# Kernel optimization log

Measured on AMD Instinct MI355X. Metric: run time of the kernel, lower is better.

The kernel has to match this reference:

```python
import jax, jax.numpy as jnp
import numpy as np

N_EMBEDDINGS = 1024
EMBEDDING_DIM = 256
DECAY = 0.99
EPSILON = 1e-05


def setup_inputs() -> dict:
    key = jax.random.key(0)
    k1, k2, k3 = jax.random.split(key, 3)
    inputs = jax.random.normal(k1, (16, 64, 64, EMBEDDING_DIM), dtype=jnp.float32)
    codebook = jax.random.normal(k2, (N_EMBEDDINGS, EMBEDDING_DIM), dtype=jnp.float32)
    ema_w = jax.random.normal(k3, (N_EMBEDDINGS, EMBEDDING_DIM), dtype=jnp.float32)
    ema_cluster_size = jnp.zeros((N_EMBEDDINGS,), dtype=jnp.float32)
    return {"inputs": inputs, "codebook": codebook, "ema_w": ema_w,
            "ema_cluster_size": ema_cluster_size}


def reference(inputs, codebook, ema_w, ema_cluster_size):
    input_shape = inputs.shape
    flat = inputs.reshape(-1, EMBEDDING_DIM)  # [N, D]
    # Squared Euclidean pairwise distances: [N, K]
    dists = (jnp.sum(flat * flat, axis=1, keepdims=True)
             + jnp.sum(codebook * codebook, axis=1)[None, :]
             - 2.0 * flat @ codebook.T)
    idx = jnp.argmin(dists, axis=1)  # [N]
    encodings = jax.nn.one_hot(idx, N_EMBEDDINGS, dtype=flat.dtype)  # [N, K]
    quantized = (encodings @ codebook).reshape(input_shape)
    # EMA updates (training mode)
    cs = ema_cluster_size * DECAY + (1.0 - DECAY) * jnp.sum(encodings, axis=0)
    n = jnp.sum(cs)
    cs = (cs + EPSILON) / (n + cs * EPSILON) * n  # faithful to original expression
    dw = encodings.T @ flat  # [K, D] scatter-accumulate via matmul
    new_ema_w = ema_w * DECAY + (1.0 - DECAY) * dw
    new_codebook = new_ema_w / cs[:, None]
    return quantized, encodings, cs, new_ema_w, new_codebook
```

## Files before the change

kernel.cpp:

```cpp
#include <hip/hip_runtime.h>

#define N_ROWS 65536
#define D 256
#define K 1024
#define DECAYF 0.99f
#define OMDF 0.01f
#define EPSF 1e-5f

typedef _Float16 f16;
typedef _Float16 f16x8 __attribute__((ext_vector_type(8)));
typedef float f32x16 __attribute__((ext_vector_type(16)));

__global__ __launch_bounds__(256) void norms_kernel(const float* __restrict__ cb,
                                                    float* __restrict__ cnorm) {
    const int row = blockIdx.x * 4 + (threadIdx.x >> 6);
    const int lane = threadIdx.x & 63;
    const float4 v = *reinterpret_cast<const float4*>(cb + row * D + lane * 4);
    float s = v.x * v.x + v.y * v.y + v.z * v.z + v.w * v.w;
    #pragma unroll
    for (int m = 32; m; m >>= 1) s += __shfl_xor(s, m);
    if (lane == 0) cnorm[row] = s;
}

__global__ __launch_bounds__(256) void split_cb_kernel(const float* __restrict__ cb,
                                                       char* __restrict__ wsB) {
    const int g = blockIdx.x * 256 + threadIdx.x;
    const int sp = g & 15;
    const int c = (g >> 4) & 255;
    const int sd = g >> 12;
    const int ct = sd >> 2, dk = sd & 3;
    const int sl = sp ^ (c & 7);
    const int v = sl >> 3, ks = (sl >> 1) & 3, h = sl & 1;
    const float* src = cb + (size_t)(ct * 256 + c) * D + dk * 64 + ks * 16 + h * 8;
    f16 out[8];
    #pragma unroll
    for (int e = 0; e < 8; ++e) {
        const float f = src[e];
        const f16 hi = (f16)f;
        out[e] = v ? (f16)(f - (float)hi) : hi;
    }
    *reinterpret_cast<f16x8*>(wsB + (size_t)g * 16) = *reinterpret_cast<f16x8*>(out);
}

__global__ __launch_bounds__(256, 2) void argmin_mfma_kernel(
        const float* __restrict__ x, const char* __restrict__ wsB,
        const float* __restrict__ cnorm, int* __restrict__ idx_out,
        float* __restrict__ counts) {
    __shared__ char smem[81920];
    char* Alds = smem;
    char* Blds = smem + 16384;
    const int tid = threadIdx.x;
    const int wave = tid >> 6;
    const int lane = tid & 63;
    const int rw = wave >> 1;
    const int cw = wave & 1;
    const int l31 = lane & 31;
    const int h = lane >> 5;
    const int n0 = blockIdx.x * 64;

    float bestv[16];
    int besti[16];
    #pragma unroll
    for (int r = 0; r < 16; ++r) { bestv[r] = 3.4e38f; besti[r] = 0; }

    const int s_row = tid >> 2;
    const int s_c4 = tid & 3;

    for (int ct = 0; ct < 4; ++ct) {
        f32x16 acc[4];
        #pragma unroll
        for (int cf = 0; cf < 4; ++cf)
            #pragma unroll
            for (int r = 0; r < 16; ++r) acc[cf][r] = 0.f;

        for (int dks = 0; dks < 4; ++dks) {
            const int dk = (ct & 1) ? (3 - dks) : dks;
            __syncthreads();
            if (!(ct > 0 && dks == 0)) {
                const float4* xs = reinterpret_cast<const float4*>(
                    x + (size_t)(n0 + s_row) * D + dk * 64 + s_c4 * 16);
                float f[16];
                {
                    const float4 f0 = xs[0], f1 = xs[1], f2 = xs[2], f3 = xs[3];
                    f[0]=f0.x; f[1]=f0.y; f[2]=f0.z; f[3]=f0.w;
                    f[4]=f1.x; f[5]=f1.y; f[6]=f1.z; f[7]=f1.w;
                    f[8]=f2.x; f[9]=f2.y; f[10]=f2.z; f[11]=f2.w;
                    f[12]=f3.x; f[13]=f3.y; f[14]=f3.z; f[15]=f3.w;
                }
                f16 hi[16], lo[16];
                #pragma unroll
                for (int e = 0; e < 16; ++e) {
                    hi[e] = (f16)f[e];
                    lo[e] = (f16)(f[e] - (float)hi[e]);
                }
                const int sw = s_row & 7;
                char* Abase = Alds + s_row * 256;
                *reinterpret_cast<f16x8*>(Abase + (((s_c4 * 2 + 0) ^ sw) * 16)) = *reinterpret_cast<f16x8*>(&hi[0]);
                *reinterpret_cast<f16x8*>(Abase + (((s_c4 * 2 + 1) ^ sw) * 16)) = *reinterpret_cast<f16x8*>(&hi[8]);
                *reinterpret_cast<f16x8*>(Abase + (((8 + s_c4 * 2 + 0) ^ sw) * 16)) = *reinterpret_cast<f16x8*>(&lo[0]);
                *reinterpret_cast<f16x8*>(Abase + (((8 + s_c4 * 2 + 1) ^ sw) * 16)) = *reinterpret_cast<f16x8*>(&lo[8]);
            }
            {
                const int4* gsrc = reinterpret_cast<const int4*>(wsB + ((size_t)(ct * 4 + dk) << 16));
                int4* ldst = reinterpret_cast<int4*>(Blds);
                #pragma unroll
                for (int i = 0; i < 16; ++i) ldst[tid + i * 256] = gsrc[tid + i * 256];
            }
            __syncthreads();
            const int arow = rw * 32 + l31;
            const int asw = arow & 7;
            #pragma unroll
            for (int ks = 0; ks < 4; ++ks) {
                const int sA = ks * 2 + h;
                const f16x8 Ah = *reinterpret_cast<const f16x8*>(Alds + arow * 256 + ((sA ^ asw) * 16));
                const f16x8 Al = *reinterpret_cast<const f16x8*>(Alds + arow * 256 + (((8 + sA) ^ asw) * 16));
                #pragma unroll
                for (int cf = 0; cf < 4; ++cf) {
                    const int bcode = cw * 128 + cf * 32 + l31;
                    const char* Bbase = Blds + bcode * 256;
                    const int bsw = bcode & 7;
                    const f16x8 Bh = *reinterpret_cast<const f16x8*>(Bbase + ((sA ^ bsw) * 16));
                    const f16x8 Bl = *reinterpret_cast<const f16x8*>(Bbase + (((8 + sA) ^ bsw) * 16));
                    acc[cf] = __builtin_amdgcn_mfma_f32_32x32x16_f16(Ah, Bh, acc[cf], 0, 0, 0);
                    acc[cf] = __builtin_amdgcn_mfma_f32_32x32x16_f16(Ah, Bl, acc[cf], 0, 0, 0);
                    acc[cf] = __builtin_amdgcn_mfma_f32_32x32x16_f16(Al, Bh, acc[cf], 0, 0, 0);
                }
            }
        }
        #pragma unroll
        for (int cf = 0; cf < 4; ++cf) {
            const int code = ct * 256 + cw * 128 + cf * 32 + l31;
            const float cn = cnorm[code];
            #pragma unroll
            for (int r = 0; r < 16; ++r) {
                const float dist = cn - 2.f * acc[cf][r];
                if (dist < bestv[r]) { bestv[r] = dist; besti[r] = code; }
            }
        }
    }
    #pragma unroll
    for (int r = 0; r < 16; ++r) {
        float v = bestv[r];
        int b = besti[r];
        #pragma unroll
        for (int m = 16; m; m >>= 1) {
            const float ov = __shfl_xor(v, m);
            const int ob = __shfl_xor(b, m);
            if (ov < v || (ov == v && ob < b)) { v = ov; b = ob; }
        }
        bestv[r] = v; besti[r] = b;
    }
    __syncthreads();
    float* Sv = reinterpret_cast<float*>(smem);
    int*   Si = reinterpret_cast<int*>(smem + 512);
    if (l31 == 0) {
        #pragma unroll
        for (int r = 0; r < 16; ++r) {
            const int row = rw * 32 + (r & 3) + 8 * (r >> 2) + 4 * h;
            Sv[cw * 64 + row] = bestv[r];
            Si[cw * 64 + row] = besti[r];
        }
    }
    __syncthreads();
    if (tid < 64) {
        const float v0 = Sv[tid], v1 = Sv[64 + tid];
        const int b0 = Si[tid], b1 = Si[64 + tid];
        const bool take1 = (v1 < v0) || (v1 == v0 && b1 < b0);
        const int b = take1 ? b1 : b0;
        idx_out[n0 + tid] = b;
        atomicAdd(&counts[b], 1.0f);
    }
}

__global__ __launch_bounds__(256) void quant_kernel(const float* __restrict__ cb,
                                                    const int* __restrict__ idx,
                                                    float* __restrict__ quant) {
    const int n = blockIdx.x * 4 + (threadIdx.x >> 6);
    const int lane = threadIdx.x & 63;
    const int i = idx[n];
    const float4 c = *reinterpret_cast<const float4*>(cb + (size_t)i * D + lane * 4);
    *reinterpret_cast<float4*>(quant + (size_t)n * D + lane * 4) = c;
}

__global__ __launch_bounds__(256) void enc_kernel(const int* __restrict__ idx,
                                                  float* __restrict__ enc) {
    const int total = N_ROWS * (K / 4);
    for (int g = blockIdx.x * blockDim.x + threadIdx.x; g < total;
         g += gridDim.x * blockDim.x) {
        const int n = g >> 8;
        const int k0 = (g & 255) * 4;
        const int i = idx[n];
        float4 v;
        v.x = (k0 == i) ? 1.f : 0.f;
        v.y = (k0 + 1 == i) ? 1.f : 0.f;
        v.z = (k0 + 2 == i) ? 1.f : 0.f;
        v.w = (k0 + 3 == i) ? 1.f : 0.f;
        *reinterpret_cast<float4*>(enc + (size_t)g * 4) = v;
    }
}

__global__ __launch_bounds__(1024) void cs_scan_kernel(const float* __restrict__ ema_cs,
                                                       const float* __restrict__ counts,
                                                       float* __restrict__ cs_out,
                                                       int* __restrict__ cursor) {
    __shared__ float red[16];
    __shared__ float n_sh;
    __shared__ int sc[1024];
    const int k = threadIdx.x;
    const float cnt = counts[k];
    const float c = ema_cs[k] * DECAYF + OMDF * cnt;
    float s = c;
    #pragma unroll
    for (int m = 32; m; m >>= 1) s += __shfl_xor(s, m);
    if ((k & 63) == 0) red[k >> 6] = s;
    const int ic = (int)cnt;
    sc[k] = ic;
    __syncthreads();
    if (k == 0) {
        float n = 0.f;
        for (int w = 0; w < 16; ++w) n += red[w];
        n_sh = n;
    }
    for (int d = 1; d < 1024; d <<= 1) {
        const int t = (k >= d) ? sc[k - d] : 0;
        __syncthreads();
        sc[k] += t;
        __syncthreads();
    }
    const float n = n_sh;
    cs_out[k] = (c + EPSF) / (n + c * EPSF) * n;
    cursor[k] = sc[k] - ic;
}

__global__ __launch_bounds__(256) void scatter_kernel(const int* __restrict__ idx,
                                                      int* __restrict__ cursor,
                                                      int* __restrict__ rowlist,
                                                      int* __restrict__ codelist) {
    const int n = blockIdx.x * 256 + threadIdx.x;
    const int i = idx[n];
    const int pos = atomicAdd(&cursor[i], 1);
    rowlist[pos] = n;
    codelist[pos] = i;
}

__global__ __launch_bounds__(256) void chunk_sum_kernel(const float* __restrict__ x,
                                                        const int* __restrict__ rowlist,
                                                        const int* __restrict__ codelist,
                                                        float* __restrict__ dw) {
    const int wave = threadIdx.x >> 6;
    const int lane = threadIdx.x & 63;
    const int p0 = blockIdx.x * 32 + wave * 8;
    int rows[8], codes[8];
    #pragma unroll
    for (int j = 0; j < 8; ++j) {
        rows[j] = rowlist[p0 + j];
        codes[j] = codelist[p0 + j];
    }
    float4 v[8];
    #pragma unroll
    for (int j = 0; j < 8; ++j)
        v[j] = *reinterpret_cast<const float4*>(x + (size_t)rows[j] * D + lane * 4);
    float4 s = v[0];
    int cur = codes[0];
    #pragma unroll
    for (int j = 1; j < 8; ++j) {
        if (codes[j] != cur) {
            float* dst = dw + (size_t)cur * D + lane * 4;
            atomicAdd(dst + 0, s.x); atomicAdd(dst + 1, s.y);
            atomicAdd(dst + 2, s.z); atomicAdd(dst + 3, s.w);
            cur = codes[j];
            s = v[j];
        } else {
            s.x += v[j].x; s.y += v[j].y; s.z += v[j].z; s.w += v[j].w;
        }
    }
    float* dst = dw + (size_t)cur * D + lane * 4;
    atomicAdd(dst + 0, s.x); atomicAdd(dst + 1, s.y);
    atomicAdd(dst + 2, s.z); atomicAdd(dst + 3, s.w);
}

__global__ __launch_bounds__(256) void ema_kernel(const float* __restrict__ ema_w,
                                                  const float* __restrict__ dw,
                                                  const float* __restrict__ cs,
                                                  float* __restrict__ w_out,
                                                  float* __restrict__ cb_out) {
    const int e4 = blockIdx.x * blockDim.x + threadIdx.x;
    const int k = e4 >> 6;
    const float csk = cs[k];
    const float4 w = *reinterpret_cast<const float4*>(ema_w + (size_t)e4 * 4);
    const float4 d = *reinterpret_cast<const float4*>(dw + (size_t)e4 * 4);
    float4 nw, nc;
    nw.x = w.x * DECAYF + OMDF * d.x;
    nw.y = w.y * DECAYF + OMDF * d.y;
    nw.z = w.z * DECAYF + OMDF * d.z;
    nw.w = w.w * DECAYF + OMDF * d.w;
    nc.x = nw.x / csk; nc.y = nw.y / csk; nc.z = nw.z / csk; nc.w = nw.w / csk;
    *reinterpret_cast<float4*>(w_out + (size_t)e4 * 4) = nw;
    *reinterpret_cast<float4*>(cb_out + (size_t)e4 * 4) = nc;
}

extern "C" void kernel_launch(void* const* d_in, const int* in_sizes, int n_in,
                              void* d_out, int out_size, void* d_ws, size_t ws_size,
                              hipStream_t stream) {
    (void)in_sizes; (void)n_in; (void)out_size; (void)ws_size;
    const float* x      = (const float*)d_in[0];
    const float* cb     = (const float*)d_in[1];
    const float* ema_w  = (const float*)d_in[2];
    const float* ema_cs = (const float*)d_in[3];

    float* out    = (float*)d_out;
    float* quant  = out;
    float* enc    = quant + 16777216;
    float* cs_out = enc + 67108864;
    float* w_out  = cs_out + 1024;
    float* cb_out = w_out + 262144;

    float* ws       = (float*)d_ws;
    float* counts   = ws;
    float* dw       = ws + 1024;
    float* cnorm    = ws + 263168;
    int*   cursor   = (int*)(ws + 264192);
    int*   idx      = (int*)(ws + 265216);
    int*   rowlist  = (int*)(ws + 330752);
    int*   codelist = (int*)(ws + 396288);
    char*  wsB      = (char*)(ws + 461824);

    hipMemsetAsync(ws, 0, (size_t)(1024 + 262144) * sizeof(float), stream);
    norms_kernel<<<K / 4, 256, 0, stream>>>(cb, cnorm);
    split_cb_kernel<<<256, 256, 0, stream>>>(cb, wsB);
    argmin_mfma_kernel<<<N_ROWS / 64, 256, 0, stream>>>(x, wsB, cnorm, idx, counts);
    quant_kernel<<<N_ROWS / 4, 256, 0, stream>>>(cb, idx, quant);
    enc_kernel<<<2048, 256, 0, stream>>>(idx, enc);
    cs_scan_kernel<<<1, 1024, 0, stream>>>(ema_cs, counts, cs_out, cursor);
    scatter_kernel<<<N_ROWS / 256, 256, 0, stream>>>(idx, cursor, rowlist, codelist);
    chunk_sum_kernel<<<2048, 256, 0, stream>>>(x, rowlist, codelist, dw);
    ema_kernel<<<65536 / 256, 256, 0, stream>>>(ema_w, dw, cs_out, w_out, cb_out);
}
```

Before: 339.8 us.

## Fuse codebook prep, one-hot and quantize writes into argmin kernel

Merges the memset, norms and fp16 split-codebook kernels into one prep kernel. The argmin kernel now writes the one-hot encodings and the gathered quantized rows directly from its LDS-held indices, which removes two launches and the re-read of idx. The cluster-size scan replaces the block-wide LDS Hillis-Steele loop with a wave-shuffle scan. In exchange, the argmin kernel's epilogue gets longer and its 256MB encoding stores are tied to that kernel's lower occupancy.

Result: slower. 347.5 us (+2.3%).

```diff
diff --git a/kernel.cpp b/kernel.cpp
--- a/kernel.cpp
+++ b/kernel.cpp
@@ -11,41 +11,49 @@
 typedef _Float16 f16x8 __attribute__((ext_vector_type(8)));
 typedef float f32x16 __attribute__((ext_vector_type(16)));
 
-__global__ __launch_bounds__(256) void norms_kernel(const float* __restrict__ cb,
-                                                    float* __restrict__ cnorm) {
-    const int row = blockIdx.x * 4 + (threadIdx.x >> 6);
-    const int lane = threadIdx.x & 63;
-    const float4 v = *reinterpret_cast<const float4*>(cb + row * D + lane * 4);
-    float s = v.x * v.x + v.y * v.y + v.z * v.z + v.w * v.w;
-    #pragma unroll
-    for (int m = 32; m; m >>= 1) s += __shfl_xor(s, m);
-    if (lane == 0) cnorm[row] = s;
-}
-
-__global__ __launch_bounds__(256) void split_cb_kernel(const float* __restrict__ cb,
-                                                       char* __restrict__ wsB) {
-    const int g = blockIdx.x * 256 + threadIdx.x;
-    const int sp = g & 15;
-    const int c = (g >> 4) & 255;
-    const int sd = g >> 12;
-    const int ct = sd >> 2, dk = sd & 3;
-    const int sl = sp ^ (c & 7);
-    const int v = sl >> 3, ks = (sl >> 1) & 3, h = sl & 1;
-    const float* src = cb + (size_t)(ct * 256 + c) * D + dk * 64 + ks * 16 + h * 8;
-    f16 out[8];
-    #pragma unroll
-    for (int e = 0; e < 8; ++e) {
-        const float f = src[e];
-        const f16 hi = (f16)f;
-        out[e] = v ? (f16)(f - (float)hi) : hi;
-    }
-    *reinterpret_cast<f16x8*>(wsB + (size_t)g * 16) = *reinterpret_cast<f16x8*>(out);
+__global__ __launch_bounds__(256) void prep_kernel(const float* __restrict__ cb,
+                                                   float* __restrict__ cnorm,
+                                                   char* __restrict__ wsB,
+                                                   float* __restrict__ dw,
+                                                   float* __restrict__ counts) {
+    const int tid = threadIdx.x;
+    const int bid = blockIdx.x;
+    const int g = bid * 256 + tid;
+    *reinterpret_cast<float4*>(dw + (size_t)g * 4) = make_float4(0.f, 0.f, 0.f, 0.f);
+    if (g < K) counts[g] = 0.f;
+    {
+        const int row = bid * 4 + (tid >> 6);
+        const int lane = tid & 63;
+        const float4 v = *reinterpret_cast<const float4*>(cb + (size_t)row * D + lane * 4);
+        float s = v.x * v.x + v.y * v.y + v.z * v.z + v.w * v.w;
+        #pragma unroll
+        for (int m = 32; m; m >>= 1) s += __shfl_xor(s, m);
+        if (lane == 0) cnorm[row] = s;
+    }
+    {
+        const int sp = g & 15;
+        const int c = (g >> 4) & 255;
+        const int sd = g >> 12;
+        const int ct = sd >> 2, dk = sd & 3;
+        const int sl = sp ^ (c & 7);
+        const int v = sl >> 3, ks = (sl >> 1) & 3, h = sl & 1;
+        const float* src = cb + (size_t)(ct * 256 + c) * D + dk * 64 + ks * 16 + h * 8;
+        f16 out[8];
+        #pragma unroll
+        for (int e = 0; e < 8; ++e) {
+            const float f = src[e];
+            const f16 hi = (f16)f;
+            out[e] = v ? (f16)(f - (float)hi) : hi;
+        }
+        *reinterpret_cast<f16x8*>(wsB + (size_t)g * 16) = *reinterpret_cast<f16x8*>(out);
+    }
 }
 
 __global__ __launch_bounds__(256, 2) void argmin_mfma_kernel(
-        const float* __restrict__ x, const char* __restrict__ wsB,
-        const float* __restrict__ cnorm, int* __restrict__ idx_out,
-        float* __restrict__ counts) {
+        const float* __restrict__ x, const float* __restrict__ cb,
+        const char* __restrict__ wsB, const float* __restrict__ cnorm,
+        int* __restrict__ idx_out, float* __restrict__ counts,
+        float* __restrict__ quant, float* __restrict__ enc) {
     __shared__ char smem[81920];
     char* Alds = smem;
     char* Blds = smem + 16384;
@@ -169,33 +177,28 @@
         const int b = take1 ? b1 : b0;
         idx_out[n0 + tid] = b;
         atomicAdd(&counts[b], 1.0f);
-    }
-}
-
-__global__ __launch_bounds__(256) void quant_kernel(const float* __restrict__ cb,
-                                                    const int* __restrict__ idx,
-                                                    float* __restrict__ quant) {
-    const int n = blockIdx.x * 4 + (threadIdx.x >> 6);
-    const int lane = threadIdx.x & 63;
-    const int i = idx[n];
-    const float4 c = *reinterpret_cast<const float4*>(cb + (size_t)i * D + lane * 4);
-    *reinterpret_cast<float4*>(quant + (size_t)n * D + lane * 4) = c;
-}
-
-__global__ __launch_bounds__(256) void enc_kernel(const int* __restrict__ idx,
-                                                  float* __restrict__ enc) {
-    const int total = N_ROWS * (K / 4);
-    for (int g = blockIdx.x * blockDim.x + threadIdx.x; g < total;
-         g += gridDim.x * blockDim.x) {
-        const int n = g >> 8;
-        const int k0 = (g & 255) * 4;
-        const int i = idx[n];
-        float4 v;
-        v.x = (k0 == i) ? 1.f : 0.f;
-        v.y = (k0 + 1 == i) ? 1.f : 0.f;
-        v.z = (k0 + 2 == i) ? 1.f : 0.f;
-        v.w = (k0 + 3 == i) ? 1.f : 0.f;
-        *reinterpret_cast<float4*>(enc + (size_t)g * 4) = v;
+        Si[tid] = b;
+    }
+    __syncthreads();
+    {
+        const int k0 = tid * 4;
+        #pragma unroll 4
+        for (int r = 0; r < 64; ++r) {
+            const int ir = Si[r];
+            float4 v;
+            v.x = (k0 == ir) ? 1.f : 0.f;
+            v.y = (k0 + 1 == ir) ? 1.f : 0.f;
+            v.z = (k0 + 2 == ir) ? 1.f : 0.f;
+            v.w = (k0 + 3 == ir) ? 1.f : 0.f;
+            *reinterpret_cast<float4*>(enc + (((size_t)(n0 + r)) << 10) + k0) = v;
+        }
+    }
+    #pragma unroll
+    for (int it = 0; it < 16; ++it) {
+        const int r = it * 4 + wave;
+        const int ir = Si[r];
+        const float4 c = *reinterpret_cast<const float4*>(cb + (size_t)ir * D + lane * 4);
+        *reinterpret_cast<float4*>(quant + (size_t)(n0 + r) * D + lane * 4) = c;
     }
 }
 
@@ -203,33 +206,46 @@
                                                        const float* __restrict__ counts,
                                                        float* __restrict__ cs_out,
                                                        int* __restrict__ cursor) {
-    __shared__ float red[16];
+    __shared__ float wsum[16];
+    __shared__ int wisum[16];
     __shared__ float n_sh;
-    __shared__ int sc[1024];
     const int k = threadIdx.x;
+    const int wid = k >> 6;
+    const int lane = k & 63;
     const float cnt = counts[k];
     const float c = ema_cs[k] * DECAYF + OMDF * cnt;
+    const int ic = (int)cnt;
+    int v = ic;
+    #pragma unroll
+    for (int d = 1; d < 64; d <<= 1) {
+        const int t = __shfl_up(v, d);
+        if (lane >= d) v += t;
+    }
     float s = c;
     #pragma unroll
     for (int m = 32; m; m >>= 1) s += __shfl_xor(s, m);
-    if ((k & 63) == 0) red[k >> 6] = s;
-    const int ic = (int)cnt;
-    sc[k] = ic;
+    if (lane == 63) wisum[wid] = v;
+    if (lane == 0) wsum[wid] = s;
     __syncthreads();
     if (k == 0) {
         float n = 0.f;
-        for (int w = 0; w < 16; ++w) n += red[w];
+        for (int w = 0; w < 16; ++w) n += wsum[w];
         n_sh = n;
     }
-    for (int d = 1; d < 1024; d <<= 1) {
-        const int t = (k >= d) ? sc[k - d] : 0;
-        __syncthreads();
-        sc[k] += t;
-        __syncthreads();
-    }
+    if (wid == 0 && lane < 16) {
+        int wv = wisum[lane];
+        #pragma unroll
+        for (int d = 1; d < 16; d <<= 1) {
+            const int t = __shfl_up(wv, d);
+            if (lane >= d) wv += t;
+        }
+        wisum[lane] = wv;
+    }
+    __syncthreads();
     const float n = n_sh;
     cs_out[k] = (c + EPSF) / (n + c * EPSF) * n;
-    cursor[k] = sc[k] - ic;
+    const int wbase = (wid == 0) ? 0 : wisum[wid - 1];
+    cursor[k] = wbase + v - ic;
 }
 
 __global__ __launch_bounds__(256) void scatter_kernel(const int* __restrict__ idx,
@@ -325,12 +341,9 @@
     int*   codelist = (int*)(ws + 396288);
     char*  wsB      = (char*)(ws + 461824);
 
-    hipMemsetAsync(ws, 0, (size_t)(1024 + 262144) * sizeof(float), stream);
-    norms_kernel<<<K / 4, 256, 0, stream>>>(cb, cnorm);
-    split_cb_kernel<<<256, 256, 0, stream>>>(cb, wsB);
-    argmin_mfma_kernel<<<N_ROWS / 64, 256, 0, stream>>>(x, wsB, cnorm, idx, counts);
-    quant_kernel<<<N_ROWS / 4, 256, 0, stream>>>(cb, idx, quant);
-    enc_kernel<<<2048, 256, 0, stream>>>(idx, enc);
+    prep_kernel<<<256, 256, 0, stream>>>(cb, cnorm, wsB, dw, counts);
+    argmin_mfma_kernel<<<N_ROWS / 64, 256, 0, stream>>>(x, cb, wsB, cnorm, idx, counts,
+                                                        quant, enc);
     cs_scan_kernel<<<1, 1024, 0, stream>>>(ema_cs, counts, cs_out, cursor);
     scatter_kernel<<<N_ROWS / 256, 256, 0, stream>>>(idx, cursor, rowlist, codelist);
     chunk_sum_kernel<<<2048, 256, 0, stream>>>(x, rowlist, codelist, dw);
```
